# Optimization experiments

Hardware: AMD Instinct MI355X
Metric: run time of the kernel (lower is better)

The kernel has to match this reference:

```python
import jax, jax.numpy as jnp
import numpy as np
from functools import reduce


def _parabolic_kernel(t, ks):
    # z_i = linspace(-ks//2 + 1, ks//2, ks); for ks=3 -> [-1, 0, 1]
    z_i = jnp.linspace(-(ks // 2) + 1 if False else (-ks) // 2 + 1, ks // 2, ks, dtype=jnp.float32)
    z_c = z_i[:, None] ** 2 + z_i[None, :] ** 2          # [ks, ks]
    z_c = z_c / z_c[0, 0]                                # normalize by corner value
    return -z_c[None, :, :] * t[:, None, None]           # [C, ks, ks]


def setup_inputs() -> dict:
    key = jax.random.key(0)
    k1, k2 = jax.random.split(key)
    B, C, H, W = 16, 128, 256, 256
    f = jax.random.normal(k1, (B, C, H, W), dtype=jnp.float32)
    t = jax.random.uniform(k2, (C,), dtype=jnp.float32)  # per-channel parabola scale
    return {"f": f, "t": t, "ks": 3, "stride": 2}


def reference(f, t, ks, stride):
    # Morphological dilation pool: out[b,c,i,j] = max_{p,q} f[b,c,i*s+p, j*s+q] + h[c,p,q]
    B, C, H, W = f.shape
    h = _parabolic_kernel(t, ks)                         # [C, ks, ks]
    out_h = (H - ks) // stride + 1
    out_w = (W - ks) // stride + 1
    shifted = []
    for p in range(ks):
        for q in range(ks):
            win = f[:, :, p:p + (out_h - 1) * stride + 1:stride,
                          q:q + (out_w - 1) * stride + 1:stride]  # [B,C,out_h,out_w]
            shifted.append(win + h[None, :, p, q, None, None])
    return reduce(jnp.maximum, shifted)
```

## Files before the change

### kernel.cpp

```cpp
#include <hip/hip_runtime.h>


constexpr int Bn = 16, Cn = 128, Hn = 256, Wn = 256;
constexpr int OH = 127, OW = 127;

__global__ __launch_bounds__(256) void pp2d_kernel(const float* __restrict__ f,
                                                   const float* __restrict__ t,
                                                   float* __restrict__ out) {
    const int bc = blockIdx.y;
    const int c  = bc & (Cn - 1);
    const int i  = blockIdx.x * blockDim.y + threadIdx.y;
    if (i >= OH) return;
    const int tx = threadIdx.x;
    const int j0 = tx * 2;
    const bool has2 = (j0 + 1) < OW;

    const float tc   = t[c];
    const float eAdd = -0.5f * tc;
    const float kAdd = -tc;

    const float* frow = f + ((size_t)bc * Hn + (size_t)(2 * i)) * Wn;
    const int c0 = 4 * tx;

    const float4 v0 = *(const float4*)(frow + c0);
    const float4 v1 = *(const float4*)(frow + Wn + c0);
    const float4 v2 = *(const float4*)(frow + 2 * Wn + c0);
    float s0 = 0.f, s1 = 0.f, s2 = 0.f;
    if (has2) {
        s0 = frow[c0 + 4];
        s1 = frow[Wn + c0 + 4];
        s2 = frow[2 * Wn + c0 + 4];
    }

    const float center0 = v1.y;
    const float edge0   = fmaxf(fmaxf(v0.y, v2.y), fmaxf(v1.x, v1.z));
    const float corn0   = fmaxf(fmaxf(v0.x, v0.z), fmaxf(v2.x, v2.z));
    const float o0 = fmaxf(center0, fmaxf(edge0 + eAdd, corn0 + kAdd));

    float* orow = out + ((size_t)bc * OH + i) * OW;
    if (has2) {
        const float center1 = v1.w;
        const float edge1   = fmaxf(fmaxf(v0.w, v2.w), fmaxf(v1.z, s1));
        const float corn1   = fmaxf(fmaxf(v0.z, s0), fmaxf(v2.z, s2));
        const float o1 = fmaxf(center1, fmaxf(edge1 + eAdd, corn1 + kAdd));
        orow[j0]     = o0;
        orow[j0 + 1] = o1;
    } else {
        orow[j0] = o0;
    }
}

extern "C" void kernel_launch(void* const* d_in, const int* in_sizes, int n_in,
                              void* d_out, int out_size, void* d_ws, size_t ws_size,
                              hipStream_t stream) {
    const float* f = (const float*)d_in[0];
    const float* t = (const float*)d_in[1];
    float* out = (float*)d_out;

    dim3 block(64, 4, 1);
    dim3 grid((OH + 3) / 4, Bn * Cn, 1);
    pp2d_kernel<<<grid, block, 0, stream>>>(f, t, out);
}
```

Baseline: 707.2 us.

## Compute two output rows per thread, shuffle halo column, use nontemporal stores

```diff
diff --git a/kernel.cpp b/kernel.cpp
--- a/kernel.cpp
+++ b/kernel.cpp
@@ -4,49 +4,64 @@
 constexpr int Bn = 16, Cn = 128, Hn = 256, Wn = 256;
 constexpr int OH = 127, OW = 127;
 
+__device__ __forceinline__ float max4(float a, float b, float c, float d) {
+    return fmaxf(fmaxf(a, b), fmaxf(c, d));
+}
+
+__device__ __forceinline__ void compute_pair(const float4& A, const float4& B, const float4& C,
+                                             float tA, float tB, float tC,
+                                             float eAdd, float kAdd,
+                                             float& o0, float& o1) {
+    o0 = fmaxf(B.y, fmaxf(max4(A.y, C.y, B.x, B.z) + eAdd,
+                          max4(A.x, A.z, C.x, C.z) + kAdd));
+    o1 = fmaxf(B.w, fmaxf(max4(A.w, C.w, B.z, tB) + eAdd,
+                          max4(A.z, tA, C.z, tC) + kAdd));
+}
+
 __global__ __launch_bounds__(256) void pp2d_kernel(const float* __restrict__ f,
                                                    const float* __restrict__ t,
                                                    float* __restrict__ out) {
     const int bc = blockIdx.y;
     const int c  = bc & (Cn - 1);
-    const int i  = blockIdx.x * blockDim.y + threadIdx.y;
-    if (i >= OH) return;
+    const int i0 = (blockIdx.x * 4 + threadIdx.y) * 2;
     const int tx = threadIdx.x;
     const int j0 = tx * 2;
-    const bool has2 = (j0 + 1) < OW;
+    const bool has2    = (j0 + 1) < OW;
+    const bool hasRow1 = (i0 + 1) < OH;
 
     const float tc   = t[c];
     const float eAdd = -0.5f * tc;
     const float kAdd = -tc;
 
-    const float* frow = f + ((size_t)bc * Hn + (size_t)(2 * i)) * Wn;
+    const float* fb = f + ((size_t)bc * Hn + (size_t)(2 * i0)) * Wn;
     const int c0 = 4 * tx;
 
-    const float4 v0 = *(const float4*)(frow + c0);
-    const float4 v1 = *(const float4*)(frow + Wn + c0);
-    const float4 v2 = *(const float4*)(frow + 2 * Wn + c0);
-    float s0 = 0.f, s1 = 0.f, s2 = 0.f;
-    if (has2) {
-        s0 = frow[c0 + 4];
-        s1 = frow[Wn + c0 + 4];
-        s2 = frow[2 * Wn + c0 + 4];
-    }
+    const size_t off3 = hasRow1 ? (size_t)(3 * Wn) : 0;
+    const float4 v0 = *(const float4*)(fb + c0);
+    const float4 v1 = *(const float4*)(fb + Wn + c0);
+    const float4 v2 = *(const float4*)(fb + 2 * Wn + c0);
+    const float4 v3 = *(const float4*)(fb + off3 + c0);
+    const float4 v4 = *(const float4*)(fb + off3 + Wn + c0);
 
-    const float center0 = v1.y;
-    const float edge0   = fmaxf(fmaxf(v0.y, v2.y), fmaxf(v1.x, v1.z));
-    const float corn0   = fmaxf(fmaxf(v0.x, v0.z), fmaxf(v2.x, v2.z));
-    const float o0 = fmaxf(center0, fmaxf(edge0 + eAdd, corn0 + kAdd));
+    const float t0 = __shfl_down(v0.x, 1);
+    const float t1 = __shfl_down(v1.x, 1);
+    const float t2 = __shfl_down(v2.x, 1);
+    const float t3 = __shfl_down(v3.x, 1);
+    const float t4 = __shfl_down(v4.x, 1);
 
-    float* orow = out + ((size_t)bc * OH + i) * OW;
-    if (has2) {
-        const float center1 = v1.w;
-        const float edge1   = fmaxf(fmaxf(v0.w, v2.w), fmaxf(v1.z, s1));
-        const float corn1   = fmaxf(fmaxf(v0.z, s0), fmaxf(v2.z, s2));
-        const float o1 = fmaxf(center1, fmaxf(edge1 + eAdd, corn1 + kAdd));
-        orow[j0]     = o0;
-        orow[j0 + 1] = o1;
-    } else {
-        orow[j0] = o0;
+    float* orow = out + ((size_t)bc * OH + i0) * OW;
+
+    float o0, o1;
+    compute_pair(v0, v1, v2, t0, t1, t2, eAdd, kAdd, o0, o1);
+    __builtin_nontemporal_store(o0, orow + j0);
+    if (has2) __builtin_nontemporal_store(o1, orow + j0 + 1);
+
+    if (hasRow1) {
+        float p0, p1;
+        compute_pair(v2, v3, v4, t2, t3, t4, eAdd, kAdd, p0, p1);
+        float* orow1 = orow + OW;
+        __builtin_nontemporal_store(p0, orow1 + j0);
+        if (has2) __builtin_nontemporal_store(p1, orow1 + j0 + 1);
     }
 }
 
@@ -58,6 +73,6 @@
     float* out = (float*)d_out;
 
     dim3 block(64, 4, 1);
-    dim3 grid((OH + 3) / 4, Bn * Cn, 1);
+    dim3 grid(16, Bn * Cn, 1);
     pp2d_kernel<<<grid, block, 0, stream>>>(f, t, out);
 }
```

New measurement: 731.6 us. 1.03x slower.
